# Kernel tuning notes

Hardware: AMD Instinct MI355X
Metric: run time of the kernel (lower is better)

The kernel has to match this reference:

```python
import jax, jax.numpy as jnp
import numpy as np
from jax.scipy.linalg import solve_triangular

B, D, NL, NH, DH = 16, 768, 12, 12, 64
P, S, LP, NC = 10, 5, 5, 100
IMG, PATCH = 224, 16
NPTOK = (IMG // PATCH) ** 2  # 196 patches
DFF = 4 * D
LOG2PI = float(np.log(2.0 * np.pi))


def setup_inputs() -> dict:
    key = jax.random.key(0)
    ks = jax.random.split(key, 12)
    s = 0.02
    inp = {}
    inp['inputs'] = jax.random.normal(ks[0], (B, 3, IMG, IMG), jnp.float32)
    inp['patch_w'] = jax.random.normal(ks[1], (D, 3, PATCH, PATCH), jnp.float32) * s
    inp['patch_b'] = jnp.zeros((D,), jnp.float32)
    inp['cls_token'] = jax.random.normal(ks[2], (1, 1, D), jnp.float32) * s
    inp['pos_embed'] = jax.random.normal(ks[3], (1, NPTOK + 1, D), jnp.float32) * s
    inp['ln1_g'] = jnp.ones((NL, D), jnp.float32)
    inp['ln1_b'] = jnp.zeros((NL, D), jnp.float32)
    inp['qkv_w'] = jax.random.normal(ks[4], (NL, D, 3 * D), jnp.float32) * s
    inp['qkv_b'] = jnp.zeros((NL, 3 * D), jnp.float32)
    inp['proj_w'] = jax.random.normal(ks[5], (NL, D, D), jnp.float32) * s
    inp['proj_b'] = jnp.zeros((NL, D), jnp.float32)
    inp['ln2_g'] = jnp.ones((NL, D), jnp.float32)
    inp['ln2_b'] = jnp.zeros((NL, D), jnp.float32)
    inp['fc1_w'] = jax.random.normal(ks[6], (NL, D, DFF), jnp.float32) * s
    inp['fc1_b'] = jnp.zeros((NL, DFF), jnp.float32)
    inp['fc2_w'] = jax.random.normal(ks[7], (NL, DFF, D), jnp.float32) * s
    inp['fc2_b'] = jnp.zeros((NL, D), jnp.float32)
    inp['norm_g'] = jnp.ones((D,), jnp.float32)
    inp['norm_b'] = jnp.zeros((D,), jnp.float32)
    inp['head_w'] = jax.random.normal(ks[8], (D, NC), jnp.float32) * s
    inp['head_b'] = jnp.zeros((NC,), jnp.float32)
    inp['prompt'] = jax.random.normal(ks[9], (P, LP, D), jnp.float32)
    m = jax.random.normal(ks[10], (P, D), jnp.float32)
    inp['mean'] = m / jnp.linalg.norm(m, axis=-1, keepdims=True)
    # init in torch: ones + eye, repeated per pool component (positive definite)
    inp['variance'] = jnp.ones((P, D, D), jnp.float32) + jnp.eye(D, dtype=jnp.float32)[None]
    return inp


def _ln(x, g, b, eps=1e-6):
    m = x.mean(-1, keepdims=True)
    v = jnp.mean((x - m) ** 2, axis=-1, keepdims=True)
    return (x - m) * jax.lax.rsqrt(v + eps) * g + b


def _blocks(x, blk):
    def step(x, pl):
        g1, b1, qw, qb, pw, pb, g2, b2, f1w, f1b, f2w, f2b = pl
        Bn, N, _ = x.shape
        h = _ln(x, g1, b1)
        qkv = (h @ qw + qb).reshape(Bn, N, 3, NH, DH).transpose(2, 0, 3, 1, 4)
        q, k, v = qkv[0], qkv[1], qkv[2]  # [B,H,N,dh]
        att = jax.nn.softmax(jnp.einsum('bhqd,bhkd->bhqk', q, k) * (1.0 / np.sqrt(DH)), axis=-1)
        o = jnp.einsum('bhqk,bhkd->bhqd', att, v).transpose(0, 2, 1, 3).reshape(Bn, N, D)
        x = x + o @ pw + pb
        h = _ln(x, g2, b2)
        return x + jax.nn.gelu(h @ f1w + f1b) @ f2w + f2b, None
    x, _ = jax.lax.scan(step, x, blk)
    return x


def _mvn_logprob(q, mean, cov):
    # q: [B,D]; mean: [P,D]; cov: [P,D,D] -> [B,P]
    L = jnp.linalg.cholesky(cov)
    diff = q[:, None, :] - mean[None]  # [B,P,D]
    y = jax.vmap(lambda Lp, dp: solve_triangular(Lp, dp.T, lower=True), in_axes=(0, 1))(L, diff)  # [P,D,B]
    quad = jnp.sum(y * y, axis=1).T  # [B,P]
    logdet = 2.0 * jnp.sum(jnp.log(jnp.diagonal(L, axis1=-2, axis2=-1)), axis=-1)  # [P]
    return -0.5 * (D * LOG2PI + logdet[None, :] + quad)


def reference(inputs, patch_w, patch_b, cls_token, pos_embed, ln1_g, ln1_b, qkv_w, qkv_b,
              proj_w, proj_b, ln2_g, ln2_b, fc1_w, fc1_b, fc2_w, fc2_b, norm_g, norm_b,
              head_w, head_b, prompt, mean, variance):
    blk = (ln1_g, ln1_b, qkv_w, qkv_b, proj_w, proj_b, ln2_g, ln2_b, fc1_w, fc1_b, fc2_w, fc2_b)
    # patch embed: conv16x16 stride16 -> [B,196,D]
    img = jax.lax.conv_general_dilated(inputs, patch_w, (PATCH, PATCH), 'VALID',
                                       dimension_numbers=('NCHW', 'OIHW', 'NCHW'))
    img = img.reshape(B, D, NPTOK).transpose(0, 2, 1) + patch_b
    t = jnp.concatenate([jnp.broadcast_to(cls_token, (B, 1, D)), img], axis=1)
    x0 = t + pos_embed
    # query pass (no_grad in original)
    q = _ln(_blocks(x0, blk), norm_g, norm_b)[:, 0]  # [B,D]
    cov = jnp.abs(variance) + jnp.eye(D, dtype=variance.dtype)[None]
    logp = _mvn_logprob(q, mean, cov)  # [B,P]
    _, topk = jax.lax.top_k(logp, S)  # [B,S]
    prompts = prompt[topk].reshape(B, S * LP, D) + pos_embed[0, 0]
    # prompted pass: [cls(+pos), prompts, raw patch tokens]
    x = jnp.concatenate([x0[:, :1], prompts, img], axis=1)  # [B, 1+S*LP+196, D]
    x = _ln(_blocks(x, blk), norm_g, norm_b)
    x = x[:, 1:S * LP + 1].mean(axis=1)  # mean over prompt tokens
    return x @ head_w + head_b  # [B,NC]
```

## Files before the change

kernel.cpp:

```cpp
#include <hip/hip_runtime.h>
#include <stdint.h>
#include <math.h>


typedef _Float16 h16_t;
typedef _Float16 h8v __attribute__((ext_vector_type(8)));
typedef _Float16 h4v __attribute__((ext_vector_type(4)));
typedef float    f4v __attribute__((ext_vector_type(4)));

#define DEV static __device__ __forceinline__

DEV float wred64(float s) {
#pragma unroll
  for (int m = 1; m < 64; m <<= 1) s += __shfl_xor(s, m, 64);
  return s;
}
DEV float gelu_f(float x) {
  float u = 0.7978845608028654f * x * (1.0f + 0.044715f * x * x);
  u = fminf(fmaxf(u, -30.0f), 30.0f);
  float e = __expf(-2.0f * u);
  return 0.5f * x * (1.0f + (1.0f - e) / (1.0f + e));
}

#define GLD16(gp, lp) __builtin_amdgcn_global_load_lds( \
  (const __attribute__((address_space(1))) unsigned int*)(const void*)(gp), \
  (__attribute__((address_space(3))) unsigned int*)(void*)(lp), 16, 0, 0)

template <int TJ>
__global__ __launch_bounds__(256) void hgemm_t(
    const h16_t* __restrict__ A, const h16_t* __restrict__ B,
    float* __restrict__ C32, h16_t* __restrict__ C16,
    const float* __restrict__ bias,
    int M, int N, int K, int lda, int ldb, int ldc32, int ldc16,
    float alpha, int act, int addC)
{
  constexpr int BN = TJ * 32;
  __shared__ __align__(16) h16_t As[128 * 32];
  __shared__ __align__(16) h16_t Bs[BN * 32];
  int tid = threadIdx.x;
  int w = tid >> 6, lane = tid & 63;
  int m0 = blockIdx.x << 7, n0 = blockIdx.y * BN;
  int qm = (w & 1) << 6, qn = (w >> 1) * (TJ * 16);
  int scol = (lane & 3) << 3;
  int fr = lane & 15, fk = (lane >> 4) << 3;

  f4v acc[4][TJ];
#pragma unroll
  for (int i = 0; i < 4; i++)
#pragma unroll
    for (int j = 0; j < TJ; j++)
#pragma unroll
      for (int r = 0; r < 4; r++) acc[i][j][r] = 0.0f;

  for (int k0 = 0; k0 < K; k0 += 32) {
    __syncthreads();
#pragma unroll
    for (int i = 0; i < 2; i++) {
      int rr = (w << 5) + (i << 4) + (lane >> 2);
      int gm = m0 + rr; gm = gm < M ? gm : M - 1;
      GLD16(A + (size_t)gm * lda + k0 + scol, &As[((w << 5) + (i << 4)) << 5]);
    }
#pragma unroll
    for (int i = 0; i < TJ / 2; i++) {
      int rb = w * (TJ / 2) * 16 + i * 16;
      int rr = rb + (lane >> 2);
      int gn = n0 + rr; gn = gn < N ? gn : N - 1;
      GLD16(B + (size_t)gn * ldb + k0 + scol, &Bs[rb << 5]);
    }
    __syncthreads();
    h8v af[4], bf[TJ];
#pragma unroll
    for (int t = 0; t < 4; t++)
      af[t] = *(const h8v*)&As[((qm + (t << 4) + fr) << 5) + fk];
#pragma unroll
    for (int t = 0; t < TJ; t++)
      bf[t] = *(const h8v*)&Bs[((qn + (t << 4) + fr) << 5) + fk];
#pragma unroll
    for (int ti = 0; ti < 4; ti++)
#pragma unroll
      for (int tj = 0; tj < TJ; tj++)
        acc[ti][tj] = __builtin_amdgcn_mfma_f32_16x16x32_f16(af[ti], bf[tj], acc[ti][tj], 0, 0, 0);
  }

  int colb = n0 + qn + fr;
  int rowb = m0 + qm + ((lane >> 4) << 2);
#pragma unroll
  for (int tj = 0; tj < TJ; tj++) {
    int col = colb + (tj << 4);
    if (col >= N) continue;
    float bv = (bias != nullptr) ? bias[col] : 0.0f;
#pragma unroll
    for (int ti = 0; ti < 4; ti++) {
#pragma unroll
      for (int rg = 0; rg < 4; rg++) {
        int row = rowb + (ti << 4) + rg;
        if (row >= M) continue;
        float v = alpha * acc[ti][tj][rg] + bv;
        if (act) v = gelu_f(v);
        if (C32) {
          size_t off = (size_t)row * ldc32 + col;
          if (addC) v += C32[off];
          C32[off] = v;
        }
        if (C16) C16[(size_t)row * ldc16 + col] = (h16_t)v;
      }
    }
  }
}

DEV void stg8(const h16_t* __restrict__ src, int row0, int rowmax, int ldk,
              char* ldsb, unsigned lbase, int tid) {
#pragma unroll
  for (int r = 0; r < 2; r++) {
    unsigned P = ((unsigned)r << 13) + ((unsigned)tid << 4);
    unsigned Q = P ^ (((P >> 7) & 3u) << 4);
    int row = (int)(Q >> 6);
    int kb = (int)((Q & 63u) >> 1);
    int gr = row0 + row; gr = gr < rowmax ? gr : rowmax - 1;
    GLD16(src + (size_t)gr * ldk + kb,
          ldsb + lbase + (r << 13) + ((tid >> 6) << 10));
  }
}

#define FENCE() asm volatile("" ::: "memory")
#define RBAR() do { FENCE(); __builtin_amdgcn_s_barrier(); FENCE(); } while (0)
#define VM8() asm volatile("s_waitcnt vmcnt(8)" ::: "memory")

#define LOADFRAGS(S, G) do { \
  unsigned ab_ = cb + ((unsigned)(S) << 14); \
  unsigned bb_ = cb + 32768u + ((unsigned)(S) << 14); \
  _Pragma("unroll") for (int t = 0; t < 4; t++) { \
    unsigned PA_ = ((unsigned)((wm << 7) + ((G) << 6) + (t << 4) + fr) << 6) + ((unsigned)quad << 4); \
    PA_ ^= ((PA_ >> 7) & 3u) << 4; \
    af[t] = *(const h8v*)(ldsb + ab_ + PA_); \
    unsigned PB_ = ((unsigned)((wn << 6) + (t << 4) + fr) << 6) + ((unsigned)quad << 4); \
    PB_ ^= ((PB_ >> 7) & 3u) << 4; \
    bf[t] = *(const h8v*)(ldsb + bb_ + PB_); \
  } } while (0)

#define MM8(G) do { \
  __builtin_amdgcn_s_setprio(1); \
  _Pragma("unroll") for (int ti = 0; ti < 4; ti++) \
  _Pragma("unroll") for (int tj = 0; tj < 4; tj++) \
    acc[((G) << 2) + ti][tj] = __builtin_amdgcn_mfma_f32_16x16x32_f16(af[ti], bf[tj], acc[((G) << 2) + ti][tj], 0, 0, 0); \
  __builtin_amdgcn_s_setprio(0); } while (0)

template <int ACT>
__global__ __launch_bounds__(512, 2) void hgemm8(
    const h16_t* __restrict__ A, const h16_t* __restrict__ B,
    h16_t* __restrict__ C16, const float* __restrict__ bias,
    int M, int N, int K, int ldc16)
{
  __shared__ __align__(16) char ldsb[131072];
  int tid = threadIdx.x;
  int w = tid >> 6, lane = tid & 63;
  int wm = w >> 2, wn = w & 3;
  int fr = lane & 15, quad = lane >> 4;
  int m0 = blockIdx.x << 8, n0 = blockIdx.y << 8;

  f4v acc[8][4];
#pragma unroll
  for (int i2 = 0; i2 < 8; i2++)
#pragma unroll
    for (int j2 = 0; j2 < 4; j2++)
#pragma unroll
      for (int r2 = 0; r2 < 4; r2++) acc[i2][j2][r2] = 0.0f;

  int NT = K >> 6;

  stg8(A,      m0, M, K, ldsb, 0u,              tid);
  stg8(B,      n0, N, K, ldsb, 32768u,          tid);
  stg8(A + 32, m0, M, K, ldsb, 16384u,          tid);
  stg8(B + 32, n0, N, K, ldsb, 32768u + 16384u, tid);
  stg8(A + 64, m0, M, K, ldsb, 65536u,          tid);
  stg8(B + 64, n0, N, K, ldsb, 65536u + 32768u, tid);
  VM8();
  __builtin_amdgcn_s_barrier();
  FENCE();

  for (int i = 0; i < NT; i++) {
    unsigned cb = (unsigned)(i & 1) << 16;
    unsigned ob = cb ^ 65536u;
    int tA = (i + 1 < NT) ? i + 1 : NT - 1;
    int tB = (i + 2 < NT) ? i + 2 : NT - 1;
    h8v af[4], bf[4];

    LOADFRAGS(0, 0);
    stg8(A + (tA << 6) + 32, m0, M, K, ldsb, ob + 16384u, tid);
    RBAR();
    MM8(0);
    RBAR();
    LOADFRAGS(0, 1);
    stg8(B + (tA << 6) + 32, n0, N, K, ldsb, ob + 49152u, tid);
    RBAR();
    MM8(1);
    VM8();
    RBAR();
    LOADFRAGS(1, 0);
    stg8(A + (tB << 6), m0, M, K, ldsb, cb, tid);
    RBAR();
    MM8(0);
    RBAR();
    LOADFRAGS(1, 1);
    stg8(B + (tB << 6), n0, N, K, ldsb, cb + 32768u, tid);
    RBAR();
    MM8(1);
    VM8();
    RBAR();
  }
  asm volatile("s_waitcnt vmcnt(0)" ::: "memory");

  int row0 = m0 + (wm << 7) + (quad << 2);
  int col0 = n0 + (wn << 6) + fr;
  float bv[4];
#pragma unroll
  for (int nj = 0; nj < 4; nj++) bv[nj] = bias[col0 + (nj << 4)];
#pragma unroll
  for (int mi = 0; mi < 8; mi++) {
#pragma unroll
    for (int rg = 0; rg < 4; rg++) {
      int row = row0 + (mi << 4) + rg;
      if (row < M) {
#pragma unroll
        for (int nj = 0; nj < 4; nj++) {
          float v = acc[mi][nj][rg] + bv[nj];
          if (ACT) v = gelu_f(v);
          C16[(size_t)row * ldc16 + col0 + (nj << 4)] = (h16_t)v;
        }
      }
    }
  }
}

__global__ __launch_bounds__(256) void flash_attn(
    const h16_t* __restrict__ qkv, h16_t* __restrict__ o, int N)
{
  int z = blockIdx.y;
  int b = z / 12, h = z - (z / 12) * 12;
  const h16_t* base = qkv + (size_t)b * N * 2304 + h * 64;
  int q0 = blockIdx.x << 6;
  int tid = threadIdx.x, w = tid >> 6, lane = tid & 63;
  int fr = lane & 15, fk = (lane >> 4) << 3;
  int quad = lane >> 4;

  __shared__ __align__(16) h16_t Qs[2][64 * 32];
  __shared__ __align__(16) h16_t Ks[2][64 * 32];
  __shared__ __align__(16) h16_t Ps[4][1024];
  __shared__ __align__(16) h16_t Vt[64 * 68];

#pragma unroll
  for (int s = 0; s < 2; s++) {
    int gq = q0 + (w << 4) + (lane >> 2); gq = gq < N ? gq : N - 1;
    GLD16(base + (size_t)gq * 2304 + (s << 5) + ((lane & 3) << 3), &Qs[s][(w << 4) << 5]);
  }
  __syncthreads();
  h8v af0 = *(const h8v*)&Qs[0][(((w << 4) + fr) << 5) + fk];
  h8v af1 = *(const h8v*)&Qs[1][(((w << 4) + fr) << 5) + fk];

  float mrow[4], lrow[4];
  f4v accO[4];
#pragma unroll
  for (int r = 0; r < 4; r++) { mrow[r] = -1e30f; lrow[r] = 0.0f; }
#pragma unroll
  for (int t = 0; t < 4; t++)
#pragma unroll
    for (int r = 0; r < 4; r++) accO[t][r] = 0.0f;

  int nj = (N + 63) >> 6;
  for (int jt = 0; jt < nj; jt++) {
    int j0 = jt << 6;
    __syncthreads();
#pragma unroll
    for (int s = 0; s < 2; s++) {
      int gj = j0 + (w << 4) + (lane >> 2); gj = gj < N ? gj : N - 1;
      GLD16(base + (size_t)gj * 2304 + 768 + (s << 5) + ((lane & 3) << 3), &Ks[s][(w << 4) << 5]);
    }
#pragma unroll
    for (int i = 0; i < 16; i++) {
      int j = (w << 4) + i;
      int gj = j0 + j; gj = gj < N ? gj : N - 1;
      Vt[lane * 68 + j] = base[(size_t)gj * 2304 + 1536 + lane];
    }
    __syncthreads();

    f4v s4[4];
#pragma unroll
    for (int t = 0; t < 4; t++) {
      h8v b0 = *(const h8v*)&Ks[0][(((t << 4) + fr) << 5) + fk];
      h8v b1 = *(const h8v*)&Ks[1][(((t << 4) + fr) << 5) + fk];
      f4v s; s[0] = s[1] = s[2] = s[3] = 0.0f;
      s = __builtin_amdgcn_mfma_f32_16x16x32_f16(af0, b0, s, 0, 0, 0);
      s = __builtin_amdgcn_mfma_f32_16x16x32_f16(af1, b1, s, 0, 0, 0);
      s4[t] = s;
    }
#pragma unroll
    for (int r = 0; r < 4; r++) {
      float tm = -1e30f;
#pragma unroll
      for (int t = 0; t < 4; t++) {
        float v = s4[t][r] * 0.125f;
        if (j0 + (t << 4) + fr >= N) v = -1e30f;
        s4[t][r] = v;
        tm = fmaxf(tm, v);
      }
#pragma unroll
      for (int m = 1; m < 16; m <<= 1) tm = fmaxf(tm, __shfl_xor(tm, m, 64));
      float mn = fmaxf(mrow[r], tm);
      float alpha = __expf(mrow[r] - mn);
      mrow[r] = mn;
      float rs = 0.0f;
#pragma unroll
      for (int t = 0; t < 4; t++) {
        float e = __expf(s4[t][r] - mn);
        s4[t][r] = e;
        rs += e;
      }
#pragma unroll
      for (int m = 1; m < 16; m <<= 1) rs += __shfl_xor(rs, m, 64);
      lrow[r] = lrow[r] * alpha + rs;
#pragma unroll
      for (int t = 0; t < 4; t++) accO[t][r] *= alpha;
#pragma unroll
      for (int t = 0; t < 4; t++)
        Ps[w][((t >> 1) << 9) + (((quad << 2) + r) << 5) + ((t & 1) << 4) + fr] = (h16_t)s4[t][r];
    }
#pragma unroll
    for (int s = 0; s < 2; s++) {
      h8v ap = *(const h8v*)&Ps[w][(s << 9) + (fr << 5) + fk];
#pragma unroll
      for (int t = 0; t < 4; t++) {
        int vidx = ((t << 4) + fr) * 68 + (s << 5) + fk;
        h4v v0 = *(const h4v*)&Vt[vidx];
        h4v v1 = *(const h4v*)&Vt[vidx + 4];
        h8v bv;
#pragma unroll
        for (int i = 0; i < 4; i++) { bv[i] = v0[i]; bv[i + 4] = v1[i]; }
        accO[t] = __builtin_amdgcn_mfma_f32_16x16x32_f16(ap, bv, accO[t], 0, 0, 0);
      }
    }
  }

#pragma unroll
  for (int r = 0; r < 4; r++) {
    int q = q0 + (w << 4) + (quad << 2) + r;
    if (q >= N) continue;
    float inv = 1.0f / lrow[r];
    h16_t* op = o + ((size_t)b * N + q) * 768 + h * 64 + fr;
#pragma unroll
    for (int t = 0; t < 4; t++) op[t << 4] = (h16_t)(accO[t][r] * inv);
  }
}

__global__ __launch_bounds__(256) void wcvt_t(const float* __restrict__ in,
                                              h16_t* __restrict__ o, int K, int N) {
  int z = blockIdx.z;
  in += (size_t)z * K * N;
  o  += (size_t)z * K * N;
  int n0 = blockIdx.x << 5, k0 = blockIdx.y << 5;
  __shared__ float t[32][33];
  int a = threadIdx.x >> 3, b4 = (threadIdx.x & 7) << 2;
  f4v v = *(const f4v*)(in + (size_t)(k0 + a) * N + n0 + b4);
  t[a][b4] = v[0]; t[a][b4 + 1] = v[1]; t[a][b4 + 2] = v[2]; t[a][b4 + 3] = v[3];
  __syncthreads();
  h4v h;
#pragma unroll
  for (int i = 0; i < 4; i++) h[i] = (h16_t)t[b4 + i][a];
  *(h4v*)(o + (size_t)(n0 + a) * K + k0 + b4) = h;
}

__global__ void cvt_flat(const float* __restrict__ in, h16_t* __restrict__ o, int n) {
  int i = blockIdx.x * 256 + threadIdx.x;
  if (i < n) o[i] = (h16_t)in[i];
}

__global__ void im2col_k(const float* __restrict__ in, h16_t* __restrict__ col) {
  int idx = blockIdx.x * 256 + threadIdx.x;
  if (idx >= 16 * 196 * 768) return;
  int k = idx % 768; int t = idx / 768; int p2 = t % 196; int b = t / 196;
  int c = k >> 8, ij = k & 255, i = ij >> 4, j = ij & 15;
  int py = p2 / 14, px = p2 % 14;
  col[idx] = (h16_t)in[(((size_t)b * 3 + c) * 224 + py * 16 + i) * 224 + px * 16 + j];
}

__global__ void build_x0_k(float* __restrict__ x, const float* __restrict__ img,
                           const float* __restrict__ cls, const float* __restrict__ pos) {
  int idx = blockIdx.x * 256 + threadIdx.x;
  if (idx >= 16 * 197 * 768) return;
  int d = idx % 768; int t = idx / 768; int n = t % 197; int b = t / 197;
  float v = (n == 0) ? cls[d] : img[((size_t)b * 196 + (n - 1)) * 768 + d];
  x[idx] = v + pos[n * 768 + d];
}

__global__ void build_x2_k(float* __restrict__ x, const float* __restrict__ img,
                           const float* __restrict__ cls, const float* __restrict__ pos,
                           const float* __restrict__ prompt, const int* __restrict__ tk) {
  int idx = blockIdx.x * 256 + threadIdx.x;
  if (idx >= 16 * 222 * 768) return;
  int d = idx % 768; int t = idx / 768; int n = t % 222; int b = t / 222;
  float v;
  if (n == 0) v = cls[d] + pos[d];
  else if (n < 26) {
    int s = (n - 1) / 5, li = (n - 1) % 5;
    v = prompt[((size_t)tk[b * 5 + s] * 5 + li) * 768 + d] + pos[d];
  } else {
    v = img[((size_t)b * 196 + (n - 26)) * 768 + d];
  }
  x[idx] = v;
}

__global__ void ln_rows(const float* __restrict__ in, h16_t* __restrict__ o16,
                        float* __restrict__ o32, const float* __restrict__ g,
                        const float* __restrict__ b, int rows, long istr, long ostr) {
  int gw = ((blockIdx.x << 8) + threadIdx.x) >> 6;
  int lane = threadIdx.x & 63;
  if (gw >= rows) return;
  const float* rp = in + (size_t)gw * istr;
  float v[12]; float s = 0;
#pragma unroll
  for (int i = 0; i < 12; i++) { v[i] = rp[lane + (i << 6)]; s += v[i]; }
  s = wred64(s);
  float mean = s * (1.0f / 768.0f);
  float s2 = 0;
#pragma unroll
  for (int i = 0; i < 12; i++) { float d = v[i] - mean; s2 += d * d; }
  s2 = wred64(s2);
  float rstd = rsqrtf(s2 * (1.0f / 768.0f) + 1e-6f);
#pragma unroll
  for (int i = 0; i < 12; i++) {
    int k = lane + (i << 6);
    float o = (v[i] - mean) * rstd * g[k] + b[k];
    if (o16) o16[(size_t)gw * ostr + k] = (h16_t)o;
    if (o32) o32[(size_t)gw * ostr + k] = o;
  }
}

__global__ void cov_init_k(const float* __restrict__ var, float* __restrict__ Lb) {
  size_t i = (size_t)blockIdx.x * 256 + threadIdx.x;
  if (i >= (size_t)10 * 589824) return;
  int ij = (int)(i % 589824);
  int r = ij / 768, c = ij - r * 768;
  Lb[i] = fabsf(var[i]) + ((r == c) ? 1.0f : 0.0f);
}

__global__ __launch_bounds__(256) void sgemm_nt_chol(float* __restrict__ Lb, int jb) {
  int p = blockIdx.z;
  float* base = Lb + (size_t)p * 589824;
  const float* A = base + (size_t)jb * 768;
  const float* Bp = A;
  float* C = base + (size_t)jb * 768 + jb;
  int m0 = blockIdx.x << 6;
  __shared__ float As[16][64];
  __shared__ float Bs[16][64];
  int tid = threadIdx.x;
  int am = tid & 63, ak = (tid >> 6) << 2;
  int tm = (tid >> 4) << 2, tn = (tid & 15) << 2;
  float acc[4][4] = {};
  for (int k0 = 0; k0 < jb; k0 += 16) {
    f4v va = *(const f4v*)(A + (size_t)(m0 + am) * 768 + k0 + ak);
    f4v vb = *(const f4v*)(Bp + (size_t)am * 768 + k0 + ak);
#pragma unroll
    for (int i = 0; i < 4; i++) { As[ak + i][am] = va[i]; Bs[ak + i][am] = vb[i]; }
    __syncthreads();
#pragma unroll
    for (int kk = 0; kk < 16; kk++) {
      f4v a = *(const f4v*)&As[kk][tm];
      f4v b = *(const f4v*)&Bs[kk][tn];
#pragma unroll
      for (int i = 0; i < 4; i++)
#pragma unroll
        for (int j = 0; j < 4; j++) acc[i][j] += a[i] * b[j];
    }
    __syncthreads();
  }
#pragma unroll
  for (int i = 0; i < 4; i++)
#pragma unroll
    for (int j = 0; j < 4; j++)
      C[(size_t)(m0 + tm + i) * 768 + tn + j] -= acc[i][j];
}

template <int CB>
DEV void chol_sub(float (&row)[64], int r, bool actv, float* Bl, float* Dg, float* Dinv) {
  if constexpr (CB > 0) {
    if (actv && r >= CB && r < CB + 16) {
      int c = r - CB;
#pragma unroll
      for (int k = 0; k < CB; k++) Bl[k * 16 + c] = row[k];
    }
    __syncthreads();
    if (actv && r >= CB) {
#pragma unroll
      for (int k = 0; k < CB; k++) {
        float a = row[k];
#pragma unroll
        for (int c = 0; c < 16; c++) row[CB + c] -= a * Bl[k * 16 + c];
      }
    }
  }
  __syncthreads();
  if (r >= CB && r < CB + 16) {
    int c = r - CB;
#pragma unroll
    for (int j = 0; j < 16; j++) {
      float dv = __shfl(row[CB + j], CB + j, 64);
      float ds = sqrtf(dv);
      float di = 1.0f / ds;
      if (c == j) row[CB + j] = ds;
      else if (c > j) row[CB + j] *= di;
#pragma unroll
      for (int c2 = j + 1; c2 < 16; c2++) {
        float lc2 = __shfl(row[CB + j], CB + c2, 64);
        if (c >= c2) row[CB + c2] -= row[CB + j] * lc2;
      }
    }
#pragma unroll
    for (int j = 0; j < 16; j++) Dg[c * 16 + j] = row[CB + j];
    Dinv[c] = 1.0f / row[CB + c];
  }
  __syncthreads();
  if (actv && r >= CB + 16) {
#pragma unroll
    for (int c2 = 0; c2 < 16; c2++) {
      float v = row[CB + c2];
#pragma unroll
      for (int k = 0; k < c2; k++) v -= row[CB + k] * Dg[c2 * 16 + k];
      row[CB + c2] = v * Dinv[c2];
    }
  }
  __syncthreads();
}

__global__ __launch_bounds__(768) void chol_panel(float* __restrict__ Lb, int jb) {
  int p = blockIdx.x;
  float* L = Lb + (size_t)p * 589824;
  int R = 768 - jb;
  int r = threadIdx.x;
  bool actv = r < R;
  __shared__ float Bl[48 * 16];
  __shared__ float Dg[256];
  __shared__ float Dinv[16];
  float row[64];
  float* my = L + (size_t)(jb + r) * 768 + jb;
  if (actv) {
#pragma unroll
    for (int i = 0; i < 16; i++) {
      f4v v = *(const f4v*)(my + 4 * i);
      row[4 * i] = v[0]; row[4 * i + 1] = v[1]; row[4 * i + 2] = v[2]; row[4 * i + 3] = v[3];
    }
  }
  chol_sub<0>(row, r, actv, Bl, Dg, Dinv);
  chol_sub<16>(row, r, actv, Bl, Dg, Dinv);
  chol_sub<32>(row, r, actv, Bl, Dg, Dinv);
  chol_sub<48>(row, r, actv, Bl, Dg, Dinv);
  if (actv) {
#pragma unroll
    for (int i = 0; i < 16; i++) {
      f4v v; v[0] = row[4 * i]; v[1] = row[4 * i + 1]; v[2] = row[4 * i + 2]; v[3] = row[4 * i + 3];
      *(f4v*)(my + 4 * i) = v;
    }
  }
}

__global__ __launch_bounds__(256) void ltrans_k(const float* __restrict__ Lb,
                                                float* __restrict__ Ut,
                                                float* __restrict__ dg) {
  int p = blockIdx.z;
  const float* L = Lb + (size_t)p * 589824;
  float* U = Ut + (size_t)p * 589824;
  int r0 = blockIdx.x << 5, c0 = blockIdx.y << 5;
  __shared__ float t[32][33];
  int a = threadIdx.x >> 3, b4 = (threadIdx.x & 7) << 2;
  f4v v = *(const f4v*)(L + (size_t)(r0 + a) * 768 + c0 + b4);
  t[a][b4] = v[0]; t[a][b4 + 1] = v[1]; t[a][b4 + 2] = v[2]; t[a][b4 + 3] = v[3];
  __syncthreads();
  int k = c0 + a;
  f4v ov;
#pragma unroll
  for (int i = 0; i < 4; i++) {
    int j = r0 + b4 + i;
    float val = t[b4 + i][a];
    ov[i] = (j > k) ? val : 0.0f;
    if (j == k) dg[p * 768 + k] = val;
  }
  *(f4v*)(U + (size_t)k * 768 + r0 + b4) = ov;
}

__global__ __launch_bounds__(64) void trsm2(const float* __restrict__ Ut,
                                            const float* __restrict__ dg,
                                            const float* __restrict__ q,
                                            const float* __restrict__ mean,
                                            float* __restrict__ logp) {
  int gw = blockIdx.x;
  int p = gw >> 4, b = gw & 15;
  const float* U = Ut + (size_t)p * 589824;
  int lane = threadIdx.x;

  float y[12], dinv[12];
  float lacc = 0.0f;
#pragma unroll
  for (int m = 0; m < 12; m++) {
    int i = lane + (m << 6);
    y[m] = q[b * 768 + i] - mean[p * 768 + i];
    float d = dg[p * 768 + i];
    dinv[m] = 1.0f / d;
    lacc += __logf(d);
  }

  float u[4][12];
#pragma unroll
  for (int d0 = 0; d0 < 4; d0++)
#pragma unroll
    for (int mm = 0; mm < 12; mm++)
      u[d0][mm] = U[(size_t)d0 * 768 + lane + (mm << 6)];

#pragma unroll
  for (int m = 0; m < 12; m++) {
    for (int kb = 0; kb < 64; kb += 4) {
#pragma unroll
      for (int kd = 0; kd < 4; kd++) {
        int k = (m << 6) + kb + kd;
        float yo = __shfl(y[m], kb + kd, 64);
        float di = __shfl(dinv[m], kb + kd, 64);
        float yk = yo * di;
        if (lane == kb + kd) y[m] = yk;
        float un[12];
        bool pf = (k + 4) < 768;
        const float* rp = U + (size_t)(k + 4) * 768 + lane;
#pragma unroll
        for (int mm = 0; mm < 12; mm++) un[mm] = pf ? rp[mm << 6] : 0.0f;
#pragma unroll
        for (int mm = 0; mm < 12; mm++) y[mm] -= u[kd][mm] * yk;
#pragma unroll
        for (int mm = 0; mm < 12; mm++) u[kd][mm] = un[mm];
      }
    }
  }

  float quad = 0.0f;
#pragma unroll
  for (int m = 0; m < 12; m++) quad += y[m] * y[m];
  quad = wred64(quad);
  lacc = wred64(lacc);
  if (lane == 0)
    logp[b * 10 + p] = -0.5f * (768.0f * 1.8378770664093453f + 2.0f * lacc + quad);
}

__global__ void topk_k(const float* __restrict__ logp, int* __restrict__ tk) {
  int b = threadIdx.x;
  if (b >= 16) return;
  float v[10];
#pragma unroll
  for (int p = 0; p < 10; p++) v[p] = logp[b * 10 + p];
#pragma unroll
  for (int s = 0; s < 5; s++) {
    int bi = 0; float bv = v[0];
#pragma unroll
    for (int p = 1; p < 10; p++) if (v[p] > bv) { bv = v[p]; bi = p; }
    tk[b * 5 + s] = bi;
    v[bi] = -3.0e38f;
  }
}

DEV float blocksum256(float s, float* red) {
  s = wred64(s);
  __syncthreads();
  if ((threadIdx.x & 63) == 0) red[threadIdx.x >> 6] = s;
  __syncthreads();
  return red[0] + red[1] + red[2] + red[3];
}

__global__ __launch_bounds__(256) void final_head(const float* __restrict__ x,
                                                  const float* __restrict__ g,
                                                  const float* __restrict__ b,
                                                  const float* __restrict__ hw,
                                                  const float* __restrict__ hb,
                                                  float* __restrict__ out) {
  int bb = blockIdx.x, tid = threadIdx.x;
  __shared__ float xm[768];
  __shared__ float red[4];
  float a0 = 0, a1 = 0, a2 = 0;
  for (int j = 1; j <= 25; j++) {
    const float* rp = x + ((size_t)bb * 222 + j) * 768;
    float v0 = rp[tid], v1 = rp[tid + 256], v2 = rp[tid + 512];
    float s = blocksum256(v0 + v1 + v2, red);
    float mean = s * (1.0f / 768.0f);
    float d0 = v0 - mean, d1 = v1 - mean, d2 = v2 - mean;
    float s2 = blocksum256(d0 * d0 + d1 * d1 + d2 * d2, red);
    float rstd = rsqrtf(s2 * (1.0f / 768.0f) + 1e-6f);
    a0 += d0 * rstd * g[tid] + b[tid];
    a1 += d1 * rstd * g[tid + 256] + b[tid + 256];
    a2 += d2 * rstd * g[tid + 512] + b[tid + 512];
  }
  xm[tid] = a0 * (1.0f / 25.0f);
  xm[tid + 256] = a1 * (1.0f / 25.0f);
  xm[tid + 512] = a2 * (1.0f / 25.0f);
  __syncthreads();
  if (tid < 100) {
    float s = hb[tid];
    for (int d = 0; d < 768; d++) s += xm[d] * hw[d * 100 + tid];
    out[bb * 100 + tid] = s;
  }
}

extern "C" void kernel_launch(void* const* d_in, const int* in_sizes, int n_in,
                              void* d_out, int out_size, void* d_ws, size_t ws_size,
                              hipStream_t stream) {
  (void)in_sizes; (void)n_in; (void)out_size; (void)ws_size;
  const float* inp     = (const float*)d_in[0];
  const float* patchw  = (const float*)d_in[1];
  const float* patchb  = (const float*)d_in[2];
  const float* cls     = (const float*)d_in[3];
  const float* pos     = (const float*)d_in[4];
  const float* ln1g    = (const float*)d_in[5];
  const float* ln1b    = (const float*)d_in[6];
  const float* qkvw    = (const float*)d_in[7];
  const float* qkvb    = (const float*)d_in[8];
  const float* projw   = (const float*)d_in[9];
  const float* projb   = (const float*)d_in[10];
  const float* ln2g    = (const float*)d_in[11];
  const float* ln2b    = (const float*)d_in[12];
  const float* fc1w    = (const float*)d_in[13];
  const float* fc1b    = (const float*)d_in[14];
  const float* fc2w    = (const float*)d_in[15];
  const float* fc2b    = (const float*)d_in[16];
  const float* normg   = (const float*)d_in[17];
  const float* normb   = (const float*)d_in[18];
  const float* headw   = (const float*)d_in[19];
  const float* headb   = (const float*)d_in[20];
  const float* prompt  = (const float*)d_in[21];
  const float* meanp   = (const float*)d_in[22];
  const float* var     = (const float*)d_in[23];
  float* out = (float*)d_out;

  char* ws = (char*)d_ws;
  size_t cur = 0;
  auto alloc = [&](size_t bytes) { size_t r = cur; cur += (bytes + 255) & ~(size_t)255; return r; };
  float* x    = (float*)(ws + alloc((size_t)3552 * 768 * 4));
  float* img  = (float*)(ws + alloc((size_t)3136 * 768 * 4));
  float* qb   = (float*)(ws + alloc((size_t)16 * 768 * 4));
  float* logp = (float*)(ws + alloc(1024));
  int*   tk   = (int*)(ws + alloc(1024));
  float* dg   = (float*)(ws + alloc((size_t)10 * 768 * 4));
  h16_t* h16   = (h16_t*)(ws + alloc((size_t)3552 * 768 * 2));
  size_t qkv_off = alloc((size_t)3552 * 2304 * 2);
  h16_t* qkv16 = (h16_t*)(ws + qkv_off);
  size_t g_off = alloc((size_t)3552 * 3072 * 2);
  h16_t* g16   = (h16_t*)(ws + g_off);
  float* Lbuf  = (float*)(ws + alloc((size_t)10 * 589824 * 4));
  h16_t* wq16  = (h16_t*)(ws + alloc((size_t)12 * 2304 * 768 * 2));
  h16_t* wp16  = (h16_t*)(ws + alloc((size_t)12 * 768 * 768 * 2));
  h16_t* w116  = (h16_t*)(ws + alloc((size_t)12 * 3072 * 768 * 2));
  h16_t* w216  = (h16_t*)(ws + alloc((size_t)12 * 768 * 3072 * 2));
  h16_t* wpt16 = (h16_t*)(ws + alloc((size_t)768 * 768 * 2));
  h16_t* col16 = (h16_t*)(ws + g_off);
  float* Ut    = (float*)(ws + qkv_off);

  wcvt_t<<<dim3(72, 24, 12), 256, 0, stream>>>(qkvw, wq16, 768, 2304);
  wcvt_t<<<dim3(24, 24, 12), 256, 0, stream>>>(projw, wp16, 768, 768);
  wcvt_t<<<dim3(96, 24, 12), 256, 0, stream>>>(fc1w, w116, 768, 3072);
  wcvt_t<<<dim3(24, 96, 12), 256, 0, stream>>>(fc2w, w216, 3072, 768);
  cvt_flat<<<2304, 256, 0, stream>>>(patchw, wpt16, 589824);

  im2col_k<<<9408, 256, 0, stream>>>(inp, col16);
  hgemm_t<2><<<dim3(25, 12), 256, 0, stream>>>(col16, wpt16, img, nullptr, patchb,
      3136, 768, 768, 768, 768, 768, 0, 1.0f, 0, 0);
  build_x0_k<<<9456, 256, 0, stream>>>(x, img, cls, pos);

  auto pass = [&](int Ntok) {
    int M = 16 * Ntok;
    int Mt = (M + 127) / 128;
    int Mt8 = (M + 255) / 256;
    int Qt = (Ntok + 63) / 64;
    for (int l = 0; l < 12; l++) {
      ln_rows<<<(M + 3) / 4, 256, 0, stream>>>(x, h16, nullptr, ln1g + l * 768, ln1b + l * 768, M, 768, 768);
      hgemm8<0><<<dim3(Mt8, 9), 512, 0, stream>>>(h16, wq16 + (size_t)l * 2304 * 768, qkv16,
          qkvb + l * 2304, M, 2304, 768, 2304);
      flash_attn<<<dim3(Qt, 192), 256, 0, stream>>>(qkv16, h16, Ntok);
      hgemm_t<2><<<dim3(Mt, 12), 256, 0, stream>>>(h16, wp16 + (size_t)l * 768 * 768, x, nullptr,
          projb + l * 768, M, 768, 768, 768, 768, 768, 0, 1.0f, 0, 1);
      ln_rows<<<(M + 3) / 4, 256, 0, stream>>>(x, h16, nullptr, ln2g + l * 768, ln2b + l * 768, M, 768, 768);
      hgemm8<1><<<dim3(Mt8, 12), 512, 0, stream>>>(h16, w116 + (size_t)l * 3072 * 768, g16,
          fc1b + l * 3072, M, 3072, 768, 3072);
      hgemm_t<2><<<dim3(Mt, 12), 256, 0, stream>>>(g16, w216 + (size_t)l * 768 * 3072, x, nullptr,
          fc2b + l * 768, M, 768, 3072, 3072, 3072, 768, 0, 1.0f, 0, 1);
    }
  };

  pass(197);
  ln_rows<<<4, 256, 0, stream>>>(x, nullptr, qb, normg, normb, 16, (long)197 * 768, 768);

  cov_init_k<<<23040, 256, 0, stream>>>(var, Lbuf);
  for (int m = 0; m < 12; m++) {
    int jb = 64 * m;
    if (m) sgemm_nt_chol<<<dim3((768 - jb) / 64, 1, 10), 256, 0, stream>>>(Lbuf, jb);
    chol_panel<<<10, 768, 0, stream>>>(Lbuf, jb);
  }
  ltrans_k<<<dim3(24, 24, 10), 256, 0, stream>>>(Lbuf, Ut, dg);
  trsm2<<<160, 64, 0, stream>>>(Ut, dg, qb, meanp, logp);
  topk_k<<<1, 64, 0, stream>>>(logp, tk);

  build_x2_k<<<10656, 256, 0, stream>>>(x, img, cls, pos, prompt, tk);
  pass(222);
  final_head<<<16, 256, 0, stream>>>(x, normg, normb, headw, headb, out);
}
```

Before: 6.565 ms.

## Add 128-row GEMM kernels for QKV, proj, fc2 and patch embed

Adds two new 512-thread MFMA GEMM kernels. hgemm8n uses a 128x256 tile for the QKV projection, and hgemm128 uses a 128x128 tile with a three-stage LDS ring and fp32 residual accumulate for proj, fc2 and patch embed. Both have launch bounds allowing two blocks per CU. The goal is better CU fill and less tail waste on the N=768 GEMMs and QKV, where the old 256-row tiles or 256-thread kernel left many CUs idle. The cost is lower per-block data reuse and more blocks loading the same weights.

```diff
diff --git a/kernel.cpp b/kernel.cpp
--- a/kernel.cpp
+++ b/kernel.cpp
@@ -108,10 +108,11 @@
   }
 }
 
-DEV void stg8(const h16_t* __restrict__ src, int row0, int rowmax, int ldk,
+template <int R>
+DEV void stgN(const h16_t* __restrict__ src, int row0, int rowmax, int ldk,
               char* ldsb, unsigned lbase, int tid) {
 #pragma unroll
-  for (int r = 0; r < 2; r++) {
+  for (int r = 0; r < R; r++) {
     unsigned P = ((unsigned)r << 13) + ((unsigned)tid << 4);
     unsigned Q = P ^ (((P >> 7) & 3u) << 4);
     int row = (int)(Q >> 6);
@@ -124,7 +125,7 @@
 
 #define FENCE() asm volatile("" ::: "memory")
 #define RBAR() do { FENCE(); __builtin_amdgcn_s_barrier(); FENCE(); } while (0)
-#define VM8() asm volatile("s_waitcnt vmcnt(8)" ::: "memory")
+#define VMW(N) asm volatile("s_waitcnt vmcnt(" #N ")" ::: "memory")
 
 #define LOADFRAGS(S, G) do { \
   unsigned ab_ = cb + ((unsigned)(S) << 14); \
@@ -168,13 +169,13 @@
 
   int NT = K >> 6;
 
-  stg8(A,      m0, M, K, ldsb, 0u,              tid);
-  stg8(B,      n0, N, K, ldsb, 32768u,          tid);
-  stg8(A + 32, m0, M, K, ldsb, 16384u,          tid);
-  stg8(B + 32, n0, N, K, ldsb, 32768u + 16384u, tid);
-  stg8(A + 64, m0, M, K, ldsb, 65536u,          tid);
-  stg8(B + 64, n0, N, K, ldsb, 65536u + 32768u, tid);
-  VM8();
+  stgN<2>(A,      m0, M, K, ldsb, 0u,              tid);
+  stgN<2>(B,      n0, N, K, ldsb, 32768u,          tid);
+  stgN<2>(A + 32, m0, M, K, ldsb, 16384u,          tid);
+  stgN<2>(B + 32, n0, N, K, ldsb, 32768u + 16384u, tid);
+  stgN<2>(A + 64, m0, M, K, ldsb, 65536u,          tid);
+  stgN<2>(B + 64, n0, N, K, ldsb, 65536u + 32768u, tid);
+  VMW(8);
   __builtin_amdgcn_s_barrier();
   FENCE();
 
@@ -186,26 +187,26 @@
     h8v af[4], bf[4];
 
     LOADFRAGS(0, 0);
-    stg8(A + (tA << 6) + 32, m0, M, K, ldsb, ob + 16384u, tid);
+    stgN<2>(A + (tA << 6) + 32, m0, M, K, ldsb, ob + 16384u, tid);
     RBAR();
     MM8(0);
     RBAR();
     LOADFRAGS(0, 1);
-    stg8(B + (tA << 6) + 32, n0, N, K, ldsb, ob + 49152u, tid);
+    stgN<2>(B + (tA << 6) + 32, n0, N, K, ldsb, ob + 49152u, tid);
     RBAR();
     MM8(1);
-    VM8();
+    VMW(8);
     RBAR();
     LOADFRAGS(1, 0);
-    stg8(A + (tB << 6), m0, M, K, ldsb, cb, tid);
+    stgN<2>(A + (tB << 6), m0, M, K, ldsb, cb, tid);
     RBAR();
     MM8(0);
     RBAR();
     LOADFRAGS(1, 1);
-    stg8(B + (tB << 6), n0, N, K, ldsb, cb + 32768u, tid);
+    stgN<2>(B + (tB << 6), n0, N, K, ldsb, cb + 32768u, tid);
     RBAR();
     MM8(1);
-    VM8();
+    VMW(8);
     RBAR();
   }
   asm volatile("s_waitcnt vmcnt(0)" ::: "memory");
@@ -226,6 +227,212 @@
           float v = acc[mi][nj][rg] + bv[nj];
           if (ACT) v = gelu_f(v);
           C16[(size_t)row * ldc16 + col0 + (nj << 4)] = (h16_t)v;
+        }
+      }
+    }
+  }
+}
+
+__global__ __launch_bounds__(512, 2) void hgemm8n(
+    const h16_t* __restrict__ A, const h16_t* __restrict__ B,
+    h16_t* __restrict__ C16, const float* __restrict__ bias,
+    int M, int N, int K, int ldc16)
+{
+  __shared__ __align__(16) char ldsb[98304];
+  int tid = threadIdx.x;
+  int w = tid >> 6, lane = tid & 63;
+  int wm = w >> 2, wn = w & 3;
+  int fr = lane & 15, quad = lane >> 4;
+  int m0 = blockIdx.x << 7, n0 = blockIdx.y << 8;
+
+  f4v acc[4][4];
+#pragma unroll
+  for (int i2 = 0; i2 < 4; i2++)
+#pragma unroll
+    for (int j2 = 0; j2 < 4; j2++)
+#pragma unroll
+      for (int r2 = 0; r2 < 4; r2++) acc[i2][j2][r2] = 0.0f;
+
+  int NT = K >> 6;
+
+  stgN<1>(A,      m0, M, K, ldsb, 0u,               tid);
+  stgN<2>(B,      n0, N, K, ldsb, 16384u,           tid);
+  stgN<1>(A + 32, m0, M, K, ldsb, 8192u,            tid);
+  stgN<2>(B + 32, n0, N, K, ldsb, 32768u,           tid);
+  stgN<1>(A + 64, m0, M, K, ldsb, 49152u,           tid);
+  stgN<2>(B + 64, n0, N, K, ldsb, 49152u + 16384u,  tid);
+  VMW(6);
+  __builtin_amdgcn_s_barrier();
+  FENCE();
+
+  for (int i = 0; i < NT; i++) {
+    unsigned cb = (i & 1) ? 49152u : 0u;
+    unsigned ob = cb ^ 49152u;
+    int tA = (i + 1 < NT) ? i + 1 : NT - 1;
+    int tB = (i + 2 < NT) ? i + 2 : NT - 1;
+    h8v af[4], bf[4];
+
+#pragma unroll
+    for (int t = 0; t < 4; t++) {
+      unsigned PA = ((unsigned)((wm << 6) + (t << 4) + fr) << 6) + ((unsigned)quad << 4);
+      PA ^= ((PA >> 7) & 3u) << 4;
+      af[t] = *(const h8v*)(ldsb + cb + PA);
+      unsigned PB = ((unsigned)((wn << 6) + (t << 4) + fr) << 6) + ((unsigned)quad << 4);
+      PB ^= ((PB >> 7) & 3u) << 4;
+      bf[t] = *(const h8v*)(ldsb + cb + 16384u + PB);
+    }
+    stgN<1>(A + (tA << 6) + 32, m0, M, K, ldsb, ob + 8192u,  tid);
+    stgN<2>(B + (tA << 6) + 32, n0, N, K, ldsb, ob + 32768u, tid);
+    RBAR();
+    __builtin_amdgcn_s_setprio(1);
+#pragma unroll
+    for (int ti = 0; ti < 4; ti++)
+#pragma unroll
+      for (int tj = 0; tj < 4; tj++)
+        acc[ti][tj] = __builtin_amdgcn_mfma_f32_16x16x32_f16(af[ti], bf[tj], acc[ti][tj], 0, 0, 0);
+    __builtin_amdgcn_s_setprio(0);
+    VMW(6);
+    RBAR();
+
+#pragma unroll
+    for (int t = 0; t < 4; t++) {
+      unsigned PA = ((unsigned)((wm << 6) + (t << 4) + fr) << 6) + ((unsigned)quad << 4);
+      PA ^= ((PA >> 7) & 3u) << 4;
+      af[t] = *(const h8v*)(ldsb + cb + 8192u + PA);
+      unsigned PB = ((unsigned)((wn << 6) + (t << 4) + fr) << 6) + ((unsigned)quad << 4);
+      PB ^= ((PB >> 7) & 3u) << 4;
+      bf[t] = *(const h8v*)(ldsb + cb + 32768u + PB);
+    }
+    stgN<1>(A + (tB << 6), m0, M, K, ldsb, cb,           tid);
+    stgN<2>(B + (tB << 6), n0, N, K, ldsb, cb + 16384u,  tid);
+    RBAR();
+    __builtin_amdgcn_s_setprio(1);
+#pragma unroll
+    for (int ti = 0; ti < 4; ti++)
+#pragma unroll
+      for (int tj = 0; tj < 4; tj++)
+        acc[ti][tj] = __builtin_amdgcn_mfma_f32_16x16x32_f16(af[ti], bf[tj], acc[ti][tj], 0, 0, 0);
+    __builtin_amdgcn_s_setprio(0);
+    VMW(6);
+    RBAR();
+  }
+  asm volatile("s_waitcnt vmcnt(0)" ::: "memory");
+
+  int row0 = m0 + (wm << 6) + (quad << 2);
+  int col0 = n0 + (wn << 6) + fr;
+  float bv[4];
+#pragma unroll
+  for (int nj = 0; nj < 4; nj++) bv[nj] = bias[col0 + (nj << 4)];
+#pragma unroll
+  for (int mi = 0; mi < 4; mi++) {
+#pragma unroll
+    for (int rg = 0; rg < 4; rg++) {
+      int row = row0 + (mi << 4) + rg;
+      if (row < M) {
+#pragma unroll
+        for (int nj = 0; nj < 4; nj++) {
+          float v = acc[mi][nj][rg] + bv[nj];
+          C16[(size_t)row * ldc16 + col0 + (nj << 4)] = (h16_t)v;
+        }
+      }
+    }
+  }
+}
+
+__global__ __launch_bounds__(512, 2) void hgemm128(
+    const h16_t* __restrict__ A, const h16_t* __restrict__ B,
+    float* __restrict__ C32, const float* __restrict__ bias,
+    int M, int N, int K, int ldc, int addC)
+{
+  __shared__ __align__(16) char ldsb[98304];
+  int tid = threadIdx.x;
+  int w = tid >> 6, lane = tid & 63;
+  int wm = w >> 2, wn = w & 3;
+  int fr = lane & 15, quad = lane >> 4;
+  int m0 = blockIdx.x << 7, n0 = blockIdx.y << 7;
+
+  f4v acc[4][2];
+#pragma unroll
+  for (int i2 = 0; i2 < 4; i2++)
+#pragma unroll
+    for (int j2 = 0; j2 < 2; j2++)
+#pragma unroll
+      for (int r2 = 0; r2 < 4; r2++) acc[i2][j2][r2] = 0.0f;
+
+  int NT = K >> 6;
+
+  stgN<1>(A,       m0, M, K, ldsb, 0u,                tid);
+  stgN<1>(A + 32,  m0, M, K, ldsb, 8192u,             tid);
+  stgN<1>(B,       n0, N, K, ldsb, 16384u,            tid);
+  stgN<1>(B + 32,  n0, N, K, ldsb, 24576u,            tid);
+  stgN<1>(A + 64,  m0, M, K, ldsb, 32768u,            tid);
+  stgN<1>(A + 96,  m0, M, K, ldsb, 32768u + 8192u,    tid);
+  stgN<1>(B + 64,  n0, N, K, ldsb, 32768u + 16384u,   tid);
+  stgN<1>(B + 96,  n0, N, K, ldsb, 32768u + 24576u,   tid);
+  VMW(4);
+  __builtin_amdgcn_s_barrier();
+  FENCE();
+
+  unsigned cb = 0u;
+  unsigned sb = 65536u;
+  for (int i = 0; i < NT; i++) {
+    int tS = (i + 2 < NT) ? i + 2 : NT - 1;
+    h8v af[2][4], bf[2][2];
+#pragma unroll
+    for (int kh = 0; kh < 2; kh++) {
+      unsigned ab = cb + ((unsigned)kh << 13);
+      unsigned bb = cb + 16384u + ((unsigned)kh << 13);
+#pragma unroll
+      for (int t = 0; t < 4; t++) {
+        unsigned PA = ((unsigned)((wm << 6) + (t << 4) + fr) << 6) + ((unsigned)quad << 4);
+        PA ^= ((PA >> 7) & 3u) << 4;
+        af[kh][t] = *(const h8v*)(ldsb + ab + PA);
+      }
+#pragma unroll
+      for (int t = 0; t < 2; t++) {
+        unsigned PB = ((unsigned)((wn << 5) + (t << 4) + fr) << 6) + ((unsigned)quad << 4);
+        PB ^= ((PB >> 7) & 3u) << 4;
+        bf[kh][t] = *(const h8v*)(ldsb + bb + PB);
+      }
+    }
+    stgN<1>(A + (tS << 6),      m0, M, K, ldsb, sb,           tid);
+    stgN<1>(A + (tS << 6) + 32, m0, M, K, ldsb, sb + 8192u,   tid);
+    stgN<1>(B + (tS << 6),      n0, N, K, ldsb, sb + 16384u,  tid);
+    stgN<1>(B + (tS << 6) + 32, n0, N, K, ldsb, sb + 24576u,  tid);
+    RBAR();
+    __builtin_amdgcn_s_setprio(1);
+#pragma unroll
+    for (int kh = 0; kh < 2; kh++)
+#pragma unroll
+      for (int ti = 0; ti < 4; ti++)
+#pragma unroll
+        for (int tj = 0; tj < 2; tj++)
+          acc[ti][tj] = __builtin_amdgcn_mfma_f32_16x16x32_f16(af[kh][ti], bf[kh][tj], acc[ti][tj], 0, 0, 0);
+    __builtin_amdgcn_s_setprio(0);
+    VMW(4);
+    RBAR();
+    cb = (cb == 65536u) ? 0u : cb + 32768u;
+    sb = (sb == 65536u) ? 0u : sb + 32768u;
+  }
+  asm volatile("s_waitcnt vmcnt(0)" ::: "memory");
+
+  int row0 = m0 + (wm << 6) + (quad << 2);
+  int col0 = n0 + (wn << 5) + fr;
+  float bv[2];
+#pragma unroll
+  for (int nj = 0; nj < 2; nj++) bv[nj] = bias[col0 + (nj << 4)];
+#pragma unroll
+  for (int mi = 0; mi < 4; mi++) {
+#pragma unroll
+    for (int rg = 0; rg < 4; rg++) {
+      int row = row0 + (mi << 4) + rg;
+      if (row < M) {
+#pragma unroll
+        for (int nj = 0; nj < 2; nj++) {
+          size_t off = (size_t)row * ldc + col0 + (nj << 4);
+          float v = acc[mi][nj][rg] + bv[nj];
+          if (addC) v += C32[off];
+          C32[off] = v;
         }
       }
     }
@@ -762,27 +969,27 @@
   cvt_flat<<<2304, 256, 0, stream>>>(patchw, wpt16, 589824);
 
   im2col_k<<<9408, 256, 0, stream>>>(inp, col16);
-  hgemm_t<2><<<dim3(25, 12), 256, 0, stream>>>(col16, wpt16, img, nullptr, patchb,
-      3136, 768, 768, 768, 768, 768, 0, 1.0f, 0, 0);
+  hgemm128<<<dim3(25, 6), 512, 0, stream>>>(col16, wpt16, img, patchb,
+      3136, 768, 768, 768, 0);
   build_x0_k<<<9456, 256, 0, stream>>>(x, img, cls, pos);
 
   auto pass = [&](int Ntok) {
     int M = 16 * Ntok;
-    int Mt = (M + 127) / 128;
+    int Mt1 = (M + 127) / 128;
     int Mt8 = (M + 255) / 256;
     int Qt = (Ntok + 63) / 64;
     for (int l = 0; l < 12; l++) {
       ln_rows<<<(M + 3) / 4, 256, 0, stream>>>(x, h16, nullptr, ln1g + l * 768, ln1b + l * 768, M, 768, 768);
-      hgemm8<0><<<dim3(Mt8, 9), 512, 0, stream>>>(h16, wq16 + (size_t)l * 2304 * 768, qkv16,
+      hgemm8n<<<dim3(Mt1, 9), 512, 0, stream>>>(h16, wq16 + (size_t)l * 2304 * 768, qkv16,
           qkvb + l * 2304, M, 2304, 768, 2304);
       flash_attn<<<dim3(Qt, 192), 256, 0, stream>>>(qkv16, h16, Ntok);
-      hgemm_t<2><<<dim3(Mt, 12), 256, 0, stream>>>(h16, wp16 + (size_t)l * 768 * 768, x, nullptr,
-          projb + l * 768, M, 768, 768, 768, 768, 768, 0, 1.0f, 0, 1);
+      hgemm128<<<dim3(Mt1, 6), 512, 0, stream>>>(h16, wp16 + (size_t)l * 768 * 768, x,
+          projb + l * 768, M, 768, 768, 768, 1);
       ln_rows<<<(M + 3) / 4, 256, 0, stream>>>(x, h16, nullptr, ln2g + l * 768, ln2b + l * 768, M, 768, 768);
       hgemm8<1><<<dim3(Mt8, 12), 512, 0, stream>>>(h16, w116 + (size_t)l * 3072 * 768, g16,
           fc1b + l * 3072, M, 3072, 768, 3072);
-      hgemm_t<2><<<dim3(Mt, 12), 256, 0, stream>>>(g16, w216 + (size_t)l * 768 * 3072, x, nullptr,
-          fc2b + l * 768, M, 768, 3072, 3072, 3072, 768, 0, 1.0f, 0, 1);
+      hgemm128<<<dim3(Mt1, 6), 512, 0, stream>>>(g16, w216 + (size_t)l * 768 * 3072, x,
+          fc2b + l * 768, M, 768, 3072, 768, 1);
     }
   };
 
```

New measurement: 5.356 ms. 18.4% less time.
